# Kernel optimization log

Measured on AMD Instinct MI355X. Metric: run time of the kernel, lower is better.

## Reference

```python
import jax, jax.numpy as jnp
import numpy as np

B, T, C = 8, 4096, 256
N_LAYER, LAYER_ID = 12, 5


def setup_inputs() -> dict:
    key = jax.random.key(0)
    ks = jax.random.split(key, 5)
    x = jax.random.normal(ks[0], (B, T, C), dtype=jnp.float32)
    scale = 1.0 / np.sqrt(C)
    Wk = jax.random.normal(ks[1], (C, C), jnp.float32) * scale
    Wv = jax.random.normal(ks[2], (C, C), jnp.float32) * scale
    Wr = jax.random.normal(ks[3], (C, C), jnp.float32) * scale
    Wo = jax.random.normal(ks[4], (C, C), jnp.float32) * scale
    # 'fancy' init from _init_weights
    ratio_0_to_1 = LAYER_ID / (N_LAYER - 1)
    h = np.arange(C, dtype=np.float64)
    decay = -5.0 + 8.0 * (h / (C - 1)) ** (0.7 + 1.3 * ratio_0_to_1)
    zigzag = ((np.arange(C) + 1) % 3 - 1) * 0.5
    first = np.log(0.3) + zigzag
    return dict(
        x=x, Wk=Wk, Wv=Wv, Wr=Wr, Wo=Wo,
        spatial_decay=jnp.asarray(decay, jnp.float32),
        spatial_first=jnp.asarray(first, jnp.float32),
        ln_w=jnp.ones((C,), jnp.float32),
        ln_b=jnp.zeros((C,), jnp.float32),
    )


def _wkv(w, u, k, v):
    # Numerically-stable RWKV WKV scan, matching wkv_cuda forward.
    # w, u: [C] (already divided by T); k, v: [B, T, C]. Returns y: [B, T, C].
    MIN_VALUE = -1e38

    def step(carry, kv):
        p, q, o = carry            # [B, C] each
        kt, vt = kv                # [B, C]
        no = jnp.maximum(o, u + kt)
        a = jnp.exp(o - no)
        b = jnp.exp(u + kt - no)
        y = (a * p + b * vt) / (a * q + b)
        no2 = jnp.maximum(w + o, kt)
        a2 = jnp.exp(w + o - no2)
        b2 = jnp.exp(kt - no2)
        return (a2 * p + b2 * vt, a2 * q + b2, no2), y

    p0 = jnp.zeros(k.shape[0:1] + k.shape[2:3], k.dtype)  # [B, C]
    q0 = jnp.zeros_like(p0)
    o0 = jnp.full_like(p0, MIN_VALUE)
    kT = jnp.swapaxes(k, 0, 1)  # [T, B, C]
    vT = jnp.swapaxes(v, 0, 1)
    _, yT = jax.lax.scan(step, (p0, q0, o0), (kT, vT))
    return jnp.swapaxes(yT, 0, 1)


def _layernorm(x, w, b, eps=1e-5):
    mu = jnp.mean(x, axis=-1, keepdims=True)
    xc = x - mu
    var = jnp.mean(xc * xc, axis=-1, keepdims=True)
    return xc * jax.lax.rsqrt(var + eps) * w + b


def reference(x, Wk, Wv, Wr, Wo, spatial_decay, spatial_first, ln_w, ln_b):
    # shift_pixel == 0 -> xk = xv = xr = x (module's own code path)
    t = x.shape[1]
    k = jnp.einsum('btc,dc->btd', x, Wk)
    v = jnp.einsum('btc,dc->btd', x, Wv)
    r = jnp.einsum('btc,dc->btd', x, Wr)
    sr = jax.nn.sigmoid(r)
    y = _wkv(spatial_decay / t, spatial_first / t, k, v)
    y = _layernorm(y, ln_w, ln_b)
    return jnp.einsum('btc,dc->btd', sr * y, Wo)
```

## Files before the change

kernel.cpp:

```cpp
#include <hip/hip_runtime.h>
#include <cstdint>
#include <cstddef>

#define B_ 8
#define T_ 4096
#define C_ 256
#define NC_ 256
#define L_ (T_ / NC_)
#define M_ (B_ * T_)

typedef float f32x4 __attribute__((ext_vector_type(4)));
typedef short bf16x8 __attribute__((ext_vector_type(8)));

__device__ __forceinline__ unsigned short f2b(float f) {
    unsigned int u = __float_as_uint(f);
    u += 0x7fffu + ((u >> 16) & 1u);
    return (unsigned short)(u >> 16);
}
__device__ __forceinline__ float b2f(unsigned short h) {
    return __uint_as_float(((unsigned int)h) << 16);
}

__global__ __launch_bounds__(256) void cvt_all(const float* __restrict__ x,
                                               const float* __restrict__ Wk,
                                               const float* __restrict__ Wv,
                                               const float* __restrict__ Wr,
                                               const float* __restrict__ Wo,
                                               unsigned short* __restrict__ xb,
                                               unsigned short* __restrict__ wb) {
    const int bid = blockIdx.x;
    const float* src;
    unsigned short* dst;
    size_t base;
    if (bid < 4096) {
        src = x; dst = xb;
        base = (size_t)bid * 2048;
    } else {
        const int r = bid - 4096;
        const int mat = r >> 5;
        src = (mat == 0) ? Wk : (mat == 1) ? Wv : (mat == 2) ? Wr : Wo;
        dst = wb + (size_t)mat * 65536;
        base = (size_t)(r & 31) * 2048;
    }
    const size_t i = base + (size_t)threadIdx.x * 8;
    float4 a = *(const float4*)(src + i);
    float4 b = *(const float4*)(src + i + 4);
    bf16x8 o;
    o[0] = (short)f2b(a.x); o[1] = (short)f2b(a.y);
    o[2] = (short)f2b(a.z); o[3] = (short)f2b(a.w);
    o[4] = (short)f2b(b.x); o[5] = (short)f2b(b.y);
    o[6] = (short)f2b(b.z); o[7] = (short)f2b(b.w);
    *(bf16x8*)(dst + i) = o;
}

__global__ __launch_bounds__(256, 3) void gemm_qkv(const unsigned short* __restrict__ A,
                                                   const unsigned short* __restrict__ w0,
                                                   const unsigned short* __restrict__ w1,
                                                   const unsigned short* __restrict__ w2,
                                                   const float* __restrict__ decay,
                                                   unsigned short* __restrict__ kb,
                                                   unsigned short* __restrict__ vb,
                                                   unsigned short* __restrict__ b2,
                                                   float* __restrict__ sp,
                                                   float* __restrict__ sq,
                                                   float* __restrict__ so) {
    __shared__ unsigned short wlds[64 * 264];
    __shared__ float stage[4][16 * 68];
    const int tid = threadIdx.x;
    const int wave = tid >> 6, lane = tid & 63;
    const int quad = lane >> 4, l16 = lane & 15;
    const int m0 = blockIdx.x * 64 + wave * 16;
    const int n0 = blockIdx.y * 64;
    float* myst = stage[wave];

    bf16x8 af[8];
    {
        const unsigned short* Ar = A + (size_t)(m0 + l16) * C_ + quad * 8;
#pragma unroll
        for (int kc = 0; kc < 8; ++kc) af[kc] = *(const bf16x8*)(Ar + kc * 32);
    }

    const int r = tid >> 5;
    const int cs = (tid & 31) * 8;

    bf16x8 tmp[8];
#pragma unroll
    for (int it = 0; it < 8; ++it)
        tmp[it] = *(const bf16x8*)(w0 + (size_t)(n0 + it * 8 + r) * C_ + cs);

    float kreg[16], vreg[16];

    for (int mat = 0; mat < 3; ++mat) {
        __syncthreads();
#pragma unroll
        for (int it = 0; it < 8; ++it)
            *(bf16x8*)(wlds + (it * 8 + r) * 264 + cs) = tmp[it];
        __syncthreads();

        if (mat < 2) {
            const unsigned short* Wn = (mat == 0) ? w1 : w2;
#pragma unroll
            for (int it = 0; it < 8; ++it)
                tmp[it] = *(const bf16x8*)(Wn + (size_t)(n0 + it * 8 + r) * C_ + cs);
        }

        f32x4 acc[4];
#pragma unroll
        for (int nt = 0; nt < 4; ++nt) acc[nt] = (f32x4){0.f, 0.f, 0.f, 0.f};
#pragma unroll
        for (int nt = 0; nt < 4; ++nt) {
            const unsigned short* wrow = wlds + (nt * 16 + l16) * 264 + quad * 8;
#pragma unroll
            for (int kc = 0; kc < 8; ++kc) {
                bf16x8 wf = *(const bf16x8*)(wrow + kc * 32);
                acc[nt] = __builtin_amdgcn_mfma_f32_16x16x32_bf16(af[kc], wf, acc[nt], 0, 0, 0);
            }
        }

#pragma unroll
        for (int nt = 0; nt < 4; ++nt)
#pragma unroll
            for (int i = 0; i < 4; ++i)
                myst[(quad * 4 + i) * 68 + nt * 16 + l16] = acc[nt][i];
#pragma unroll
        for (int rr = 0; rr < 4; ++rr) {
            const int row = rr * 4 + quad;
            float4 t4 = *(const float4*)&myst[row * 68 + l16 * 4];
            const size_t gidx = (size_t)(m0 + row) * C_ + n0 + l16 * 4;
            ushort4 s4;
            if (mat == 2) {
                s4.x = f2b(1.f / (1.f + __expf(-t4.x)));
                s4.y = f2b(1.f / (1.f + __expf(-t4.y)));
                s4.z = f2b(1.f / (1.f + __expf(-t4.z)));
                s4.w = f2b(1.f / (1.f + __expf(-t4.w)));
                *(ushort4*)(b2 + gidx) = s4;
            } else {
                s4.x = f2b(t4.x); s4.y = f2b(t4.y);
                s4.z = f2b(t4.z); s4.w = f2b(t4.w);
                unsigned short* Fb = (mat == 0) ? kb : vb;
                *(ushort4*)(Fb + gidx) = s4;
            }
        }

        if (mat == 0) {
#pragma unroll
            for (int j = 0; j < L_; ++j) kreg[j] = b2f(f2b(myst[j * 68 + lane]));
        } else if (mat == 1) {
#pragma unroll
            for (int j = 0; j < L_; ++j) vreg[j] = b2f(f2b(myst[j * 68 + lane]));
            const int ch = n0 + lane;
            const float w = decay[ch] * (1.0f / T_);
            float p = 0.f, q = 0.f, o = -1e38f;
#pragma unroll
            for (int j = 0; j < L_; ++j) {
                float wo = w + o;
                float no = fmaxf(wo, kreg[j]);
                float a2 = __expf(wo - no), b2s = __expf(kreg[j] - no);
                p = a2 * p + b2s * vreg[j];
                q = a2 * q + b2s;
                o = no;
            }
            const int bb = m0 / T_;
            const int chunk = (m0 % T_) / L_;
            const size_t idx = ((size_t)bb * NC_ + chunk) * C_ + ch;
            sp[idx] = p; sq[idx] = q; so[idx] = o;
        }
    }
}

__global__ __launch_bounds__(256, 3) void gemm_out(const unsigned short* __restrict__ A,
                                                   const unsigned short* __restrict__ w0,
                                                   float* __restrict__ f0) {
    __shared__ unsigned short wlds[64 * 264];
    __shared__ float stage[4][16 * 68];
    const int tid = threadIdx.x;
    const int wave = tid >> 6, lane = tid & 63;
    const int quad = lane >> 4, l16 = lane & 15;
    const int m0 = blockIdx.x * 64 + wave * 16;
    float* myst = stage[wave];

    bf16x8 af[8];
    {
        const unsigned short* Ar = A + (size_t)(m0 + l16) * C_ + quad * 8;
#pragma unroll
        for (int kc = 0; kc < 8; ++kc) af[kc] = *(const bf16x8*)(Ar + kc * 32);
    }

    const int r = tid >> 5;
    const int cs = (tid & 31) * 8;

    bf16x8 tmp[8];
#pragma unroll
    for (int it = 0; it < 8; ++it)
        tmp[it] = *(const bf16x8*)(w0 + (size_t)(it * 8 + r) * C_ + cs);

    for (int s = 0; s < 4; ++s) {
        const int n0 = s * 64;
        __syncthreads();
#pragma unroll
        for (int it = 0; it < 8; ++it)
            *(bf16x8*)(wlds + (it * 8 + r) * 264 + cs) = tmp[it];
        __syncthreads();

        if (s < 3) {
#pragma unroll
            for (int it = 0; it < 8; ++it)
                tmp[it] = *(const bf16x8*)(w0 + (size_t)(n0 + 64 + it * 8 + r) * C_ + cs);
        }

        f32x4 acc[4];
#pragma unroll
        for (int nt = 0; nt < 4; ++nt) acc[nt] = (f32x4){0.f, 0.f, 0.f, 0.f};
#pragma unroll
        for (int nt = 0; nt < 4; ++nt) {
            const unsigned short* wrow = wlds + (nt * 16 + l16) * 264 + quad * 8;
#pragma unroll
            for (int kc = 0; kc < 8; ++kc) {
                bf16x8 wf = *(const bf16x8*)(wrow + kc * 32);
                acc[nt] = __builtin_amdgcn_mfma_f32_16x16x32_bf16(af[kc], wf, acc[nt], 0, 0, 0);
            }
        }

#pragma unroll
        for (int nt = 0; nt < 4; ++nt)
#pragma unroll
            for (int i = 0; i < 4; ++i)
                myst[(quad * 4 + i) * 68 + nt * 16 + l16] = acc[nt][i];
#pragma unroll
        for (int rr = 0; rr < 4; ++rr) {
            const int row = rr * 4 + quad;
            float4 t4 = *(const float4*)&myst[row * 68 + l16 * 4];
            *(float4*)(f0 + (size_t)(m0 + row) * C_ + n0 + l16 * 4) = t4;
        }
    }
}

__global__ __launch_bounds__(256) void wkv_combine_par(const float* __restrict__ decay,
                                                       float* __restrict__ sp,
                                                       float* __restrict__ sq,
                                                       float* __restrict__ so) {
    __shared__ float tp[16][17], tq[16][17], to[16][17];
    const int tid = threadIdx.x;
    const int cgi = tid >> 4;
    const int cl = tid & 15;
    const int b = blockIdx.x;
    const int c = blockIdx.y * 16 + cl;
    const float wL = decay[c] * (1.0f / T_) * (float)L_;
    const float wL16 = wL * 16.0f;
    const size_t base = ((size_t)b * NC_ + (size_t)cgi * 16) * C_ + c;

    float p = 0.f, q = 0.f, o = -1e38f;
#pragma unroll 4
    for (int j = 0; j < 16; ++j) {
        size_t idx = base + (size_t)j * C_;
        float lp = sp[idx], lq = sq[idx], lo = so[idx];
        float ow = o + wL;
        float no = fmaxf(ow, lo);
        float ea = __expf(ow - no), eb = __expf(lo - no);
        p = ea * p + eb * lp;
        q = ea * q + eb * lq;
        o = no;
    }
    tp[cgi][cl] = p; tq[cgi][cl] = q; to[cgi][cl] = o;

    float ip = p, iq = q, io = o;
#pragma unroll
    for (int off = 1; off < 16; off <<= 1) {
        __syncthreads();
        float ap = 0.f, aq = 0.f, ao = 0.f;
        const bool doit = (cgi >= off);
        if (doit) { ap = tp[cgi - off][cl]; aq = tq[cgi - off][cl]; ao = to[cgi - off][cl]; }
        __syncthreads();
        if (doit) {
            float ow = ao + (float)off * wL16;
            float no = fmaxf(ow, io);
            float ea = __expf(ow - no), eb = __expf(io - no);
            ip = ea * ap + eb * ip;
            iq = ea * aq + eb * iq;
            io = no;
            tp[cgi][cl] = ip; tq[cgi][cl] = iq; to[cgi][cl] = io;
        }
    }
    __syncthreads();

    float ep, eq, eo;
    if (cgi == 0) { ep = 0.f; eq = 0.f; eo = -1e38f; }
    else          { ep = tp[cgi - 1][cl]; eq = tq[cgi - 1][cl]; eo = to[cgi - 1][cl]; }

    for (int j = 0; j < 16; ++j) {
        size_t idx = base + (size_t)j * C_;
        float lp = sp[idx], lq = sq[idx], lo = so[idx];
        sp[idx] = ep; sq[idx] = eq; so[idx] = eo;
        float ow = eo + wL;
        float no = fmaxf(ow, lo);
        float ea = __expf(ow - no), eb = __expf(lo - no);
        ep = ea * ep + eb * lp;
        eq = ea * eq + eb * lq;
        eo = no;
    }
}

__global__ __launch_bounds__(256, 8) void wkv_pass2_ln(const unsigned short* __restrict__ k,
                                                       const unsigned short* __restrict__ v,
                                                       const unsigned short* __restrict__ sr,
                                                       const float* __restrict__ decay,
                                                       const float* __restrict__ first,
                                                       const float* __restrict__ lw,
                                                       const float* __restrict__ lb,
                                                       const float* __restrict__ sp,
                                                       const float* __restrict__ sq,
                                                       const float* __restrict__ so,
                                                       unsigned short* __restrict__ z) {
    __shared__ float tile[16][264];
    __shared__ float mu_s[16], rs_s[16];
    const int c = threadIdx.x, chunk = blockIdx.x, b = blockIdx.y;
    const int wave = c >> 6, lane = c & 63;
    const float w = decay[c] * (1.0f / T_);
    const float u = first[c] * (1.0f / T_);
    const float gw = lw[c], gb = lb[c];
    size_t sidx = ((size_t)b * NC_ + chunk) * C_ + c;
    float p = sp[sidx], q = sq[sidx], o = so[sidx];
    size_t base = ((size_t)b * T_ + (size_t)chunk * L_) * C_ + c;

    for (int t = 0; t < L_; t += 8) {
        float kk[8], vv[8];
#pragma unroll
        for (int j = 0; j < 8; ++j) {
            kk[j] = b2f(k[base + (size_t)(t + j) * C_]);
            vv[j] = b2f(v[base + (size_t)(t + j) * C_]);
        }
#pragma unroll
        for (int j = 0; j < 8; ++j) {
            float uk = u + kk[j];
            float no = fmaxf(o, uk);
            float a = __expf(o - no), bb = __expf(uk - no);
            tile[t + j][c] = (a * p + bb * vv[j]) / (a * q + bb);
            float wo = w + o;
            float no2 = fmaxf(wo, kk[j]);
            float a2 = __expf(wo - no2), b2 = __expf(kk[j] - no2);
            p = a2 * p + b2 * vv[j];
            q = a2 * q + b2;
            o = no2;
        }
    }
    __syncthreads();
#pragma unroll
    for (int r = 0; r < 4; ++r) {
        const int j = wave * 4 + r;
        float4 t4 = *(const float4*)&tile[j][lane * 4];
        float s = t4.x + t4.y + t4.z + t4.w;
        float ss = t4.x * t4.x + t4.y * t4.y + t4.z * t4.z + t4.w * t4.w;
#pragma unroll
        for (int m = 1; m < 64; m <<= 1) {
            s += __shfl_xor(s, m, 64);
            ss += __shfl_xor(ss, m, 64);
        }
        if (lane == 0) {
            float mu = s * (1.f / C_);
            mu_s[j] = mu;
            rs_s[j] = rsqrtf(ss * (1.f / C_) - mu * mu + 1e-5f);
        }
    }
    __syncthreads();
#pragma unroll
    for (int j = 0; j < L_; ++j) {
        float zz = (tile[j][c] - mu_s[j]) * rs_s[j] * gw + gb;
        zz *= b2f(sr[base + (size_t)j * C_]);
        z[base + (size_t)j * C_] = f2b(zz);
    }
}

extern "C" void kernel_launch(void* const* d_in, const int* in_sizes, int n_in,
                              void* d_out, int out_size, void* d_ws, size_t ws_size,
                              hipStream_t stream) {
    const float* x     = (const float*)d_in[0];
    const float* Wk    = (const float*)d_in[1];
    const float* Wv    = (const float*)d_in[2];
    const float* Wr    = (const float*)d_in[3];
    const float* Wo    = (const float*)d_in[4];
    const float* decay = (const float*)d_in[5];
    const float* first = (const float*)d_in[6];
    const float* lnw   = (const float*)d_in[7];
    const float* lnb   = (const float*)d_in[8];
    float* out = (float*)d_out;

    char* ws = (char*)d_ws;
    const size_t NE = (size_t)M_ * C_;
    unsigned short* wb  = (unsigned short*)ws; ws += 4 * 65536 * 2;
    unsigned short* xb  = (unsigned short*)ws; ws += NE * 2;
    unsigned short* kbuf = (unsigned short*)ws; ws += NE * 2;
    unsigned short* vbuf = (unsigned short*)ws; ws += NE * 2;
    unsigned short* srb = (unsigned short*)ws; ws += NE * 2;
    unsigned short* zb  = (unsigned short*)ws; ws += NE * 2;
    const size_t SE = (size_t)B_ * NC_ * C_;
    float* sp = (float*)ws; ws += SE * 4;
    float* sq = (float*)ws; ws += SE * 4;
    float* so = (float*)ws; ws += SE * 4;
    unsigned short* wkb = wb;
    unsigned short* wvb = wb + 65536;
    unsigned short* wrb = wb + 2 * 65536;
    unsigned short* wob = wb + 3 * 65536;

    cvt_all<<<4096 + 128, 256, 0, stream>>>(x, Wk, Wv, Wr, Wo, xb, wb);

    gemm_qkv<<<dim3(M_ / 64, 4), 256, 0, stream>>>(xb, wkb, wvb, wrb, decay,
                                                   kbuf, vbuf, srb, sp, sq, so);

    wkv_combine_par<<<dim3(B_, C_ / 16), 256, 0, stream>>>(decay, sp, sq, so);
    wkv_pass2_ln<<<dim3(NC_, B_), 256, 0, stream>>>(kbuf, vbuf, srb, decay, first,
                                                    lnw, lnb, sp, sq, so, zb);

    gemm_out<<<dim3(M_ / 64), 256, 0, stream>>>(zb, wob, out);
}
```

Baseline: 159.6 us.

## Fuse x bf16 conversion into QKV GEMM and loop all column slices per block

Drops the separate fp32-to-bf16 pass over x and instead converts x rows directly inside gemm_qkv when loading A fragments. Each block now iterates over all four 64-column slices instead of launching four blocks per row tile, so x is read once per row tile rather than four times. This removes the bf16 x round trip through global memory. In exchange the grid shrinks to 512 blocks with four times the serial work each, which may reduce parallelism and latency hiding.

```diff
diff --git a/kernel.cpp b/kernel.cpp
--- a/kernel.cpp
+++ b/kernel.cpp
@@ -21,28 +21,16 @@
     return __uint_as_float(((unsigned int)h) << 16);
 }
 
-__global__ __launch_bounds__(256) void cvt_all(const float* __restrict__ x,
-                                               const float* __restrict__ Wk,
-                                               const float* __restrict__ Wv,
-                                               const float* __restrict__ Wr,
-                                               const float* __restrict__ Wo,
-                                               unsigned short* __restrict__ xb,
-                                               unsigned short* __restrict__ wb) {
-    const int bid = blockIdx.x;
-    const float* src;
-    unsigned short* dst;
-    size_t base;
-    if (bid < 4096) {
-        src = x; dst = xb;
-        base = (size_t)bid * 2048;
-    } else {
-        const int r = bid - 4096;
-        const int mat = r >> 5;
-        src = (mat == 0) ? Wk : (mat == 1) ? Wv : (mat == 2) ? Wr : Wo;
-        dst = wb + (size_t)mat * 65536;
-        base = (size_t)(r & 31) * 2048;
-    }
-    const size_t i = base + (size_t)threadIdx.x * 8;
+__global__ __launch_bounds__(256) void cvt_w(const float* __restrict__ Wk,
+                                             const float* __restrict__ Wv,
+                                             const float* __restrict__ Wr,
+                                             const float* __restrict__ Wo,
+                                             unsigned short* __restrict__ wb) {
+    const int r = blockIdx.x;
+    const int mat = r >> 5;
+    const float* src = (mat == 0) ? Wk : (mat == 1) ? Wv : (mat == 2) ? Wr : Wo;
+    unsigned short* dst = wb + (size_t)mat * 65536;
+    const size_t i = (size_t)(r & 31) * 2048 + (size_t)threadIdx.x * 8;
     float4 a = *(const float4*)(src + i);
     float4 b = *(const float4*)(src + i + 4);
     bf16x8 o;
@@ -53,7 +41,7 @@
     *(bf16x8*)(dst + i) = o;
 }
 
-__global__ __launch_bounds__(256, 3) void gemm_qkv(const unsigned short* __restrict__ A,
+__global__ __launch_bounds__(256, 3) void gemm_qkv(const float* __restrict__ x,
                                                    const unsigned short* __restrict__ w0,
                                                    const unsigned short* __restrict__ w1,
                                                    const unsigned short* __restrict__ w2,
@@ -70,14 +58,22 @@
     const int wave = tid >> 6, lane = tid & 63;
     const int quad = lane >> 4, l16 = lane & 15;
     const int m0 = blockIdx.x * 64 + wave * 16;
-    const int n0 = blockIdx.y * 64;
     float* myst = stage[wave];
 
     bf16x8 af[8];
     {
-        const unsigned short* Ar = A + (size_t)(m0 + l16) * C_ + quad * 8;
-#pragma unroll
-        for (int kc = 0; kc < 8; ++kc) af[kc] = *(const bf16x8*)(Ar + kc * 32);
+        const float* Ar = x + (size_t)(m0 + l16) * C_ + quad * 8;
+#pragma unroll
+        for (int kc = 0; kc < 8; ++kc) {
+            float4 a = *(const float4*)(Ar + kc * 32);
+            float4 b = *(const float4*)(Ar + kc * 32 + 4);
+            bf16x8 o;
+            o[0] = (short)f2b(a.x); o[1] = (short)f2b(a.y);
+            o[2] = (short)f2b(a.z); o[3] = (short)f2b(a.w);
+            o[4] = (short)f2b(b.x); o[5] = (short)f2b(b.y);
+            o[6] = (short)f2b(b.z); o[7] = (short)f2b(b.w);
+            af[kc] = o;
+        }
     }
 
     const int r = tid >> 5;
@@ -86,84 +82,88 @@
     bf16x8 tmp[8];
 #pragma unroll
     for (int it = 0; it < 8; ++it)
-        tmp[it] = *(const bf16x8*)(w0 + (size_t)(n0 + it * 8 + r) * C_ + cs);
+        tmp[it] = *(const bf16x8*)(w0 + (size_t)(it * 8 + r) * C_ + cs);
 
     float kreg[16], vreg[16];
 
-    for (int mat = 0; mat < 3; ++mat) {
-        __syncthreads();
-#pragma unroll
-        for (int it = 0; it < 8; ++it)
-            *(bf16x8*)(wlds + (it * 8 + r) * 264 + cs) = tmp[it];
-        __syncthreads();
-
-        if (mat < 2) {
-            const unsigned short* Wn = (mat == 0) ? w1 : w2;
+    for (int s = 0; s < 4; ++s) {
+        const int n0 = s * 64;
+        for (int mat = 0; mat < 3; ++mat) {
+            __syncthreads();
 #pragma unroll
             for (int it = 0; it < 8; ++it)
-                tmp[it] = *(const bf16x8*)(Wn + (size_t)(n0 + it * 8 + r) * C_ + cs);
-        }
-
-        f32x4 acc[4];
-#pragma unroll
-        for (int nt = 0; nt < 4; ++nt) acc[nt] = (f32x4){0.f, 0.f, 0.f, 0.f};
-#pragma unroll
-        for (int nt = 0; nt < 4; ++nt) {
-            const unsigned short* wrow = wlds + (nt * 16 + l16) * 264 + quad * 8;
-#pragma unroll
-            for (int kc = 0; kc < 8; ++kc) {
-                bf16x8 wf = *(const bf16x8*)(wrow + kc * 32);
-                acc[nt] = __builtin_amdgcn_mfma_f32_16x16x32_bf16(af[kc], wf, acc[nt], 0, 0, 0);
+                *(bf16x8*)(wlds + (it * 8 + r) * 264 + cs) = tmp[it];
+            __syncthreads();
+
+            if (!(s == 3 && mat == 2)) {
+                const unsigned short* Wn = (mat == 0) ? w1 : (mat == 1) ? w2 : w0;
+                const int nn = (mat == 2) ? n0 + 64 : n0;
+#pragma unroll
+                for (int it = 0; it < 8; ++it)
+                    tmp[it] = *(const bf16x8*)(Wn + (size_t)(nn + it * 8 + r) * C_ + cs);
             }
-        }
-
-#pragma unroll
-        for (int nt = 0; nt < 4; ++nt)
-#pragma unroll
-            for (int i = 0; i < 4; ++i)
-                myst[(quad * 4 + i) * 68 + nt * 16 + l16] = acc[nt][i];
-#pragma unroll
-        for (int rr = 0; rr < 4; ++rr) {
-            const int row = rr * 4 + quad;
-            float4 t4 = *(const float4*)&myst[row * 68 + l16 * 4];
-            const size_t gidx = (size_t)(m0 + row) * C_ + n0 + l16 * 4;
-            ushort4 s4;
-            if (mat == 2) {
-                s4.x = f2b(1.f / (1.f + __expf(-t4.x)));
-                s4.y = f2b(1.f / (1.f + __expf(-t4.y)));
-                s4.z = f2b(1.f / (1.f + __expf(-t4.z)));
-                s4.w = f2b(1.f / (1.f + __expf(-t4.w)));
-                *(ushort4*)(b2 + gidx) = s4;
-            } else {
-                s4.x = f2b(t4.x); s4.y = f2b(t4.y);
-                s4.z = f2b(t4.z); s4.w = f2b(t4.w);
-                unsigned short* Fb = (mat == 0) ? kb : vb;
-                *(ushort4*)(Fb + gidx) = s4;
+
+            f32x4 acc[4];
+#pragma unroll
+            for (int nt = 0; nt < 4; ++nt) acc[nt] = (f32x4){0.f, 0.f, 0.f, 0.f};
+#pragma unroll
+            for (int nt = 0; nt < 4; ++nt) {
+                const unsigned short* wrow = wlds + (nt * 16 + l16) * 264 + quad * 8;
+#pragma unroll
+                for (int kc = 0; kc < 8; ++kc) {
+                    bf16x8 wf = *(const bf16x8*)(wrow + kc * 32);
+                    acc[nt] = __builtin_amdgcn_mfma_f32_16x16x32_bf16(af[kc], wf, acc[nt], 0, 0, 0);
+                }
             }
-        }
-
-        if (mat == 0) {
-#pragma unroll
-            for (int j = 0; j < L_; ++j) kreg[j] = b2f(f2b(myst[j * 68 + lane]));
-        } else if (mat == 1) {
-#pragma unroll
-            for (int j = 0; j < L_; ++j) vreg[j] = b2f(f2b(myst[j * 68 + lane]));
-            const int ch = n0 + lane;
-            const float w = decay[ch] * (1.0f / T_);
-            float p = 0.f, q = 0.f, o = -1e38f;
-#pragma unroll
-            for (int j = 0; j < L_; ++j) {
-                float wo = w + o;
-                float no = fmaxf(wo, kreg[j]);
-                float a2 = __expf(wo - no), b2s = __expf(kreg[j] - no);
-                p = a2 * p + b2s * vreg[j];
-                q = a2 * q + b2s;
-                o = no;
+
+#pragma unroll
+            for (int nt = 0; nt < 4; ++nt)
+#pragma unroll
+                for (int i = 0; i < 4; ++i)
+                    myst[(quad * 4 + i) * 68 + nt * 16 + l16] = acc[nt][i];
+#pragma unroll
+            for (int rr = 0; rr < 4; ++rr) {
+                const int row = rr * 4 + quad;
+                float4 t4 = *(const float4*)&myst[row * 68 + l16 * 4];
+                const size_t gidx = (size_t)(m0 + row) * C_ + n0 + l16 * 4;
+                ushort4 s4;
+                if (mat == 2) {
+                    s4.x = f2b(1.f / (1.f + __expf(-t4.x)));
+                    s4.y = f2b(1.f / (1.f + __expf(-t4.y)));
+                    s4.z = f2b(1.f / (1.f + __expf(-t4.z)));
+                    s4.w = f2b(1.f / (1.f + __expf(-t4.w)));
+                    *(ushort4*)(b2 + gidx) = s4;
+                } else {
+                    s4.x = f2b(t4.x); s4.y = f2b(t4.y);
+                    s4.z = f2b(t4.z); s4.w = f2b(t4.w);
+                    unsigned short* Fb = (mat == 0) ? kb : vb;
+                    *(ushort4*)(Fb + gidx) = s4;
+                }
             }
-            const int bb = m0 / T_;
-            const int chunk = (m0 % T_) / L_;
-            const size_t idx = ((size_t)bb * NC_ + chunk) * C_ + ch;
-            sp[idx] = p; sq[idx] = q; so[idx] = o;
+
+            if (mat == 0) {
+#pragma unroll
+                for (int j = 0; j < L_; ++j) kreg[j] = b2f(f2b(myst[j * 68 + lane]));
+            } else if (mat == 1) {
+#pragma unroll
+                for (int j = 0; j < L_; ++j) vreg[j] = b2f(f2b(myst[j * 68 + lane]));
+                const int ch = n0 + lane;
+                const float w = decay[ch] * (1.0f / T_);
+                float p = 0.f, q = 0.f, o = -1e38f;
+#pragma unroll
+                for (int j = 0; j < L_; ++j) {
+                    float wo = w + o;
+                    float no = fmaxf(wo, kreg[j]);
+                    float a2 = __expf(wo - no), b2s = __expf(kreg[j] - no);
+                    p = a2 * p + b2s * vreg[j];
+                    q = a2 * q + b2s;
+                    o = no;
+                }
+                const int bb = m0 / T_;
+                const int chunk = (m0 % T_) / L_;
+                const size_t idx = ((size_t)bb * NC_ + chunk) * C_ + ch;
+                sp[idx] = p; sq[idx] = q; so[idx] = o;
+            }
         }
     }
 }
@@ -387,7 +387,6 @@
     char* ws = (char*)d_ws;
     const size_t NE = (size_t)M_ * C_;
     unsigned short* wb  = (unsigned short*)ws; ws += 4 * 65536 * 2;
-    unsigned short* xb  = (unsigned short*)ws; ws += NE * 2;
     unsigned short* kbuf = (unsigned short*)ws; ws += NE * 2;
     unsigned short* vbuf = (unsigned short*)ws; ws += NE * 2;
     unsigned short* srb = (unsigned short*)ws; ws += NE * 2;
@@ -401,10 +400,10 @@
     unsigned short* wrb = wb + 2 * 65536;
     unsigned short* wob = wb + 3 * 65536;
 
-    cvt_all<<<4096 + 128, 256, 0, stream>>>(x, Wk, Wv, Wr, Wo, xb, wb);
-
-    gemm_qkv<<<dim3(M_ / 64, 4), 256, 0, stream>>>(xb, wkb, wvb, wrb, decay,
-                                                   kbuf, vbuf, srb, sp, sq, so);
+    cvt_w<<<128, 256, 0, stream>>>(Wk, Wv, Wr, Wo, wb);
+
+    gemm_qkv<<<dim3(M_ / 64), 256, 0, stream>>>(x, wkb, wvb, wrb, decay,
+                                                kbuf, vbuf, srb, sp, sq, so);
 
     wkv_combine_par<<<dim3(B_, C_ / 16), 256, 0, stream>>>(decay, sp, sq, so);
     wkv_pass2_ln<<<dim3(NC_, B_), 256, 0, stream>>>(kbuf, vbuf, srb, decay, first,
```

New measurement: 157.3 us (median of 2 runs). About the same (-1.4%).
